# Kernel tuning notes

Measured on AMD Instinct MI355X. Metric: run time of the kernel, lower is better.

Reference implementation:

```python
import jax, jax.numpy as jnp
import numpy as np


def setup_inputs() -> dict:
    key = jax.random.key(0)
    k1, k2 = jax.random.split(key)
    B, L, D = 8, 2048, 128
    query = jax.random.normal(k1, (B, L, D), dtype=jnp.float32)
    value = jax.random.normal(k2, (B, L, D), dtype=jnp.float32)
    return {"query": query, "value": value}


def reference(query, value):
    # scores: [B, Lq, Lk] = query @ value^T (note: NO 1/sqrt(d) scaling, key == value)
    scores = jnp.einsum("bqd,bkd->bqk", query, value)
    weights = jax.nn.softmax(scores, axis=-1)
    # context: [B, Lq, D]
    context = jnp.einsum("bqk,bkd->bqd", weights, value)
    return context
```

## Files before the change

### kernel.cpp

```cpp
#include <hip/hip_runtime.h>
#include <hip/hip_fp16.h>

typedef _Float16 f16;
typedef __attribute__((ext_vector_type(8))) _Float16 f16x8;
typedef __attribute__((ext_vector_type(4))) _Float16 f16x4;
typedef __attribute__((ext_vector_type(4))) short s16x4;
typedef __attribute__((ext_vector_type(4))) float f32x4;
typedef __attribute__((ext_vector_type(2))) float f32x2;

#define MFMA16(a,b,c) __builtin_amdgcn_mfma_f32_16x16x32_f16(a,b,c,0,0,0)

#define B_DIM 8
#define L_DIM 2048
#define D_DIM 128
#define NGRP 4
#define KVB 64
#define NTILES 8
#define TILE_B 16384
#define P_ST 72
#define SLAB_ST 132
#define SMEM_B 137216

__device__ __forceinline__ unsigned ldsa(const void* p) {
    return (unsigned)(unsigned long long)(const __attribute__((address_space(3))) char*)p;
}

#define TRRD(d, a, O) asm volatile("ds_read_b64_tr_b16 %0, %1 offset:" O : "=v"(d) : "v"(a))
#define LGKM0() do { asm volatile("s_waitcnt lgkmcnt(0)" ::: "memory"); __builtin_amdgcn_sched_barrier(0); } while (0)

#define PVND(TL, TH, PA0, PA1, ND) { \
    union { s16x4 s2[2]; f16x8 v; } uu; uu.s2[0] = TL; uu.s2[1] = TH; \
    acc[0][ND] = MFMA16(PA0, uu.v, acc[0][ND]); \
    acc[1][ND] = MFMA16(PA1, uu.v, acc[1][ND]); }

#define PV_HALF(AREG, PA0, PA1, S0,S0b,S1,S1b,S2,S2b,S3,S3b, NDB) { \
    s16x4 t0l,t0h,t1l,t1h,t2l,t2h,t3l,t3h; \
    TRRD(t0l, AREG, S0);  TRRD(t0h, AREG, S0b); \
    TRRD(t1l, AREG, S1);  TRRD(t1h, AREG, S1b); \
    TRRD(t2l, AREG, S2);  TRRD(t2h, AREG, S2b); \
    TRRD(t3l, AREG, S3);  TRRD(t3h, AREG, S3b); \
    LGKM0(); \
    PVND(t0l, t0h, PA0, PA1, NDB+0); PVND(t1l, t1h, PA0, PA1, NDB+1); \
    PVND(t2l, t2h, PA0, PA1, NDB+2); PVND(t3l, t3h, PA0, PA1, NDB+3); }

__global__ __launch_bounds__(512, 2) void attn_fwd(
    const float* __restrict__ Q, const float* __restrict__ V, float* __restrict__ Out)
{
    __shared__ __align__(16) char smem[SMEM_B];

    const int tid  = threadIdx.x;
    const int wv   = tid >> 6;
    const int grp  = wv >> 1;
    const int qw   = wv & 1;
    const int lane = tid & 63;
    const int lrow = lane & 15;
    const int g    = lane >> 4;

    const int blk = blockIdx.x;
    const int b   = blk & 7;
    const int q0  = (blk >> 3) * 64;

    char* grpbase = smem + grp * (2 * TILE_B);

    f16x8 qhi[2][4], qlo[2][4];
    {
        const float* qb = Q + ((size_t)b * L_DIM + q0 + qw * 32) * D_DIM;
        #pragma unroll
        for (int q2 = 0; q2 < 2; ++q2) {
            const float* qp = qb + (size_t)(q2 * 16 + lrow) * D_DIM + g * 8;
            #pragma unroll
            for (int dt = 0; dt < 4; ++dt) {
                f32x4 f0 = *(const f32x4*)(qp + dt * 32);
                f32x4 f1 = *(const f32x4*)(qp + dt * 32 + 4);
                #pragma unroll
                for (int i = 0; i < 4; ++i) {
                    f16 h0 = (f16)f0[i];
                    qhi[q2][dt][i] = h0;
                    qlo[q2][dt][i] = (f16)(f0[i] - (float)h0);
                    f16 h1 = (f16)f1[i];
                    qhi[q2][dt][i + 4] = h1;
                    qlo[q2][dt][i + 4] = (f16)(f1[i] - (float)h1);
                }
            }
        }
    }

    f32x4 acc[2][8];
    #pragma unroll
    for (int q2 = 0; q2 < 2; ++q2)
        #pragma unroll
        for (int i = 0; i < 8; ++i) acc[q2][i] = (f32x4)0.0f;
    float m_run[2] = { -3.0e38f, -3.0e38f }, l_run[2] = { 0.0f, 0.0f };

    const int kvl = qw * 32 + (lane >> 3);
    const int d4l = lane & 7;
    const int gl_off = kvl * D_DIM + d4l * 4;
    const int wbase = ((kvl >> 2) * 1024) + ((d4l >> 2) * 128) + (kvl & 3) * 32 + (d4l & 3) * 8;
    const int qkoff = (lrow >> 2) * 1024 + (g >> 1) * 128 + (lrow & 3) * 32 + (g & 1) * 16;

    const float* vb = V + ((size_t)b * L_DIM + grp * (L_DIM / NGRP)) * D_DIM;

    {
        const float* vsrc = vb + gl_off;
        f32x4 ld0[16];
        #pragma unroll
        for (int ith = 0; ith < 4; ++ith)
            #pragma unroll
            for (int itd = 0; itd < 4; ++itd)
                ld0[ith * 4 + itd] = *(const f32x4*)(vsrc + ith * 1024 + itd * 32);
        #pragma unroll
        for (int ith = 0; ith < 4; ++ith)
            #pragma unroll
            for (int itd = 0; itd < 4; ++itd) {
                f32x4 f = ld0[ith * 4 + itd];
                f16x4 hv = { (f16)f[0], (f16)f[1], (f16)f[2], (f16)f[3] };
                *(f16x4*)(grpbase + wbase + ith * 2048 + itd * 256) = hv;
            }
    }
    __syncthreads();

    for (int t = 0; t < NTILES; ++t) {
        const int c = t & 1;
        char* cur = grpbase + c * TILE_B;
        char* alt = grpbase + (c ^ 1) * TILE_B;
        const bool hn = (t + 1 < NTILES);
        const float* vnext = vb + (size_t)(t + 1) * KVB * D_DIM + gl_off;

        f32x4 ldA[8], ldB[8];
        if (hn) {
            #pragma unroll
            for (int ith = 0; ith < 2; ++ith)
                #pragma unroll
                for (int itd = 0; itd < 4; ++itd)
                    ldA[ith * 4 + itd] = *(const f32x4*)(vnext + ith * 1024 + itd * 32);
        }

        f32x4 s[2][4];
        #pragma unroll
        for (int q2 = 0; q2 < 2; ++q2)
            #pragma unroll
            for (int nt = 0; nt < 4; ++nt) s[q2][nt] = (f32x4)0.0f;
        #pragma unroll
        for (int nt = 0; nt < 4; ++nt) {
            #pragma unroll
            for (int dt = 0; dt < 4; ++dt) {
                f16x8 a = *(const f16x8*)(cur + qkoff + nt * 4096 + dt * 256);
                s[0][nt] = MFMA16(a, qhi[0][dt], s[0][nt]);
                s[0][nt] = MFMA16(a, qlo[0][dt], s[0][nt]);
                s[1][nt] = MFMA16(a, qhi[1][dt], s[1][nt]);
                s[1][nt] = MFMA16(a, qlo[1][dt], s[1][nt]);
            }
        }

        if (hn) {
            #pragma unroll
            for (int ith = 0; ith < 2; ++ith)
                #pragma unroll
                for (int itd = 0; itd < 4; ++itd)
                    ldB[ith * 4 + itd] = *(const f32x4*)(vnext + (ith + 2) * 1024 + itd * 32);
        }

        float pm[2];
        #pragma unroll
        for (int q2 = 0; q2 < 2; ++q2) {
            float tm = s[q2][0][0];
            #pragma unroll
            for (int nt = 0; nt < 4; ++nt)
                #pragma unroll
                for (int r = 0; r < 4; ++r) tm = fmaxf(tm, s[q2][nt][r]);
            tm = fmaxf(tm, __shfl_xor(tm, 16));
            tm = fmaxf(tm, __shfl_xor(tm, 32));
            pm[q2] = tm;
        }
        bool need = (pm[0] > m_run[0] + 8.0f) || (pm[1] > m_run[1] + 8.0f);
        if (__any(need)) {
            float mnew[2], scl[2];
            #pragma unroll
            for (int q2 = 0; q2 < 2; ++q2) {
                mnew[q2] = fmaxf(m_run[q2], pm[q2]);
                scl[q2]  = __expf(m_run[q2] - mnew[q2]);
                m_run[q2] = mnew[q2];
                l_run[q2] *= scl[q2];
            }
            float sr[2][4];
            #pragma unroll
            for (int r = 0; r < 4; ++r) {
                sr[0][r] = __shfl(scl[0], g * 4 + r);
                sr[1][r] = __shfl(scl[1], g * 4 + r);
            }
            #pragma unroll
            for (int q2 = 0; q2 < 2; ++q2)
                #pragma unroll
                for (int nd = 0; nd < 8; ++nd)
                    #pragma unroll
                    for (int r = 0; r < 4; ++r) acc[q2][nd][r] *= sr[q2][r];
        }
        #pragma unroll
        for (int q2 = 0; q2 < 2; ++q2) {
            float ps = 0.0f;
            #pragma unroll
            for (int nt = 0; nt < 4; ++nt)
                #pragma unroll
                for (int r = 0; r < 4; ++r) {
                    float p = __expf(s[q2][nt][r] - m_run[q2]);
                    s[q2][nt][r] = p;
                    ps += p;
                }
            ps += __shfl_xor(ps, 16);
            ps += __shfl_xor(ps, 32);
            l_run[q2] += ps;
        }

        f16* pls = (f16*)(alt + qw * 8192);
        #pragma unroll
        for (int q2 = 0; q2 < 2; ++q2) {
            #pragma unroll
            for (int nt = 0; nt < 4; ++nt) {
                f16x4 w = { (f16)s[q2][nt][0], (f16)s[q2][nt][1],
                            (f16)s[q2][nt][2], (f16)s[q2][nt][3] };
                *(f16x4*)(pls + (size_t)(q2 * 16 + lrow) * P_ST + nt * 16 + g * 4) = w;
            }
        }
        f16x8 pa00, pa01, pa10, pa11;
        pa00 = *(const f16x8*)(pls + (size_t)(lrow) * P_ST + g * 8);
        pa01 = *(const f16x8*)(pls + (size_t)(lrow) * P_ST + 32 + g * 8);
        pa10 = *(const f16x8*)(pls + (size_t)(16 + lrow) * P_ST + g * 8);
        pa11 = *(const f16x8*)(pls + (size_t)(16 + lrow) * P_ST + 32 + g * 8);

        if (hn) {
            #pragma unroll
            for (int ith = 0; ith < 2; ++ith)
                #pragma unroll
                for (int itd = 0; itd < 4; ++itd) {
                    f32x4 f = ldA[ith * 4 + itd];
                    f16x4 hv = { (f16)f[0], (f16)f[1], (f16)f[2], (f16)f[3] };
                    *(f16x4*)(alt + wbase + ith * 2048 + itd * 256) = hv;
                }
        }

        unsigned atr0 = ldsa(cur) + (unsigned)(g * 2048 + lrow * 8);
        unsigned atr1 = atr0 + 8192u;
        PV_HALF(atr0, pa00, pa10, "0","1024","128","1152","256","1280","384","1408", 0);
        PV_HALF(atr0, pa00, pa10, "512","1536","640","1664","768","1792","896","1920", 4);
        PV_HALF(atr1, pa01, pa11, "0","1024","128","1152","256","1280","384","1408", 0);
        PV_HALF(atr1, pa01, pa11, "512","1536","640","1664","768","1792","896","1920", 4);

        if (hn) {
            #pragma unroll
            for (int ith = 0; ith < 2; ++ith)
                #pragma unroll
                for (int itd = 0; itd < 4; ++itd) {
                    f32x4 f = ldB[ith * 4 + itd];
                    f16x4 hv = { (f16)f[0], (f16)f[1], (f16)f[2], (f16)f[3] };
                    *(f16x4*)(alt + wbase + (ith + 2) * 2048 + itd * 256) = hv;
                }
        }
        __syncthreads();
    }

    float* slab = (float*)smem;
    float* mlp  = (float*)(smem + 8 * 32 * SLAB_ST * 4);
    #pragma unroll
    for (int q2 = 0; q2 < 2; ++q2)
        #pragma unroll
        for (int nd = 0; nd < 8; ++nd)
            #pragma unroll
            for (int r = 0; r < 4; ++r)
                slab[(size_t)(wv * 32 + q2 * 16 + g * 4 + r) * SLAB_ST + nd * 16 + lrow] = acc[q2][nd][r];
    if (g == 0) {
        #pragma unroll
        for (int q2 = 0; q2 < 2; ++q2) {
            mlp[wv * 64 + q2 * 16 + lrow]      = m_run[q2];
            mlp[wv * 64 + 32 + q2 * 16 + lrow] = l_run[q2];
        }
    }
    __syncthreads();

    #pragma unroll
    for (int rr = 0; rr < 8; ++rr) {
        int row = wv * 8 + rr;
        int qws = row >> 5, ql = row & 31;
        float mg[4], M = -3.0e38f;
        #pragma unroll
        for (int gg = 0; gg < 4; ++gg) {
            mg[gg] = mlp[(gg * 2 + qws) * 64 + ql];
            M = fmaxf(M, mg[gg]);
        }
        float L = 0.0f, f[4];
        #pragma unroll
        for (int gg = 0; gg < 4; ++gg) {
            f[gg] = __expf(mg[gg] - M);
            L += f[gg] * mlp[(gg * 2 + qws) * 64 + 32 + ql];
        }
        float inv = 1.0f / L;
        f32x2 o = { 0.0f, 0.0f };
        #pragma unroll
        for (int gg = 0; gg < 4; ++gg) {
            f32x2 v = *(const f32x2*)&slab[(size_t)((gg * 2 + qws) * 32 + ql) * SLAB_ST + lane * 2];
            o[0] += f[gg] * v[0];
            o[1] += f[gg] * v[1];
        }
        o[0] *= inv; o[1] *= inv;
        *(f32x2*)&Out[((size_t)b * L_DIM + q0 + row) * D_DIM + lane * 2] = o;
    }
}

extern "C" void kernel_launch(void* const* d_in, const int* in_sizes, int n_in,
                              void* d_out, int out_size, void* d_ws, size_t ws_size,
                              hipStream_t stream) {
    const float* Q = (const float*)d_in[0];
    const float* V = (const float*)d_in[1];
    float* Out     = (float*)d_out;
    attn_fwd<<<dim3(B_DIM * (L_DIM / 64)), dim3(512), 0, stream>>>(Q, V, Out);
}
```

Before: 45.59 us.

## Pad LDS tile blocks, fold log2e into Q, raise MFMA priority

```diff
diff --git a/kernel.cpp b/kernel.cpp
--- a/kernel.cpp
+++ b/kernel.cpp
@@ -9,6 +9,8 @@
 typedef __attribute__((ext_vector_type(2))) float f32x2;
 
 #define MFMA16(a,b,c) __builtin_amdgcn_mfma_f32_16x16x32_f16(a,b,c,0,0,0)
+#define EXP2(x) __builtin_amdgcn_exp2f(x)
+#define LOG2E 1.4426950408889634f
 
 #define B_DIM 8
 #define L_DIM 2048
@@ -16,7 +18,8 @@
 #define NGRP 4
 #define KVB 64
 #define NTILES 8
-#define TILE_B 16384
+#define BLKB 1040
+#define TILE_B (16 * BLKB)
 #define P_ST 72
 #define SLAB_ST 132
 #define SMEM_B 137216
@@ -40,8 +43,10 @@
     TRRD(t2l, AREG, S2);  TRRD(t2h, AREG, S2b); \
     TRRD(t3l, AREG, S3);  TRRD(t3h, AREG, S3b); \
     LGKM0(); \
+    __builtin_amdgcn_s_setprio(1); \
     PVND(t0l, t0h, PA0, PA1, NDB+0); PVND(t1l, t1h, PA0, PA1, NDB+1); \
-    PVND(t2l, t2h, PA0, PA1, NDB+2); PVND(t3l, t3h, PA0, PA1, NDB+3); }
+    PVND(t2l, t2h, PA0, PA1, NDB+2); PVND(t3l, t3h, PA0, PA1, NDB+3); \
+    __builtin_amdgcn_s_setprio(0); }
 
 __global__ __launch_bounds__(512, 2) void attn_fwd(
     const float* __restrict__ Q, const float* __restrict__ V, float* __restrict__ Out)
@@ -74,12 +79,14 @@
                 f32x4 f1 = *(const f32x4*)(qp + dt * 32 + 4);
                 #pragma unroll
                 for (int i = 0; i < 4; ++i) {
-                    f16 h0 = (f16)f0[i];
+                    float s0 = f0[i] * LOG2E;
+                    f16 h0 = (f16)s0;
                     qhi[q2][dt][i] = h0;
-                    qlo[q2][dt][i] = (f16)(f0[i] - (float)h0);
-                    f16 h1 = (f16)f1[i];
+                    qlo[q2][dt][i] = (f16)(s0 - (float)h0);
+                    float s1 = f1[i] * LOG2E;
+                    f16 h1 = (f16)s1;
                     qhi[q2][dt][i + 4] = h1;
-                    qlo[q2][dt][i + 4] = (f16)(f1[i] - (float)h1);
+                    qlo[q2][dt][i + 4] = (f16)(s1 - (float)h1);
                 }
             }
         }
@@ -95,8 +102,8 @@
     const int kvl = qw * 32 + (lane >> 3);
     const int d4l = lane & 7;
     const int gl_off = kvl * D_DIM + d4l * 4;
-    const int wbase = ((kvl >> 2) * 1024) + ((d4l >> 2) * 128) + (kvl & 3) * 32 + (d4l & 3) * 8;
-    const int qkoff = (lrow >> 2) * 1024 + (g >> 1) * 128 + (lrow & 3) * 32 + (g & 1) * 16;
+    const int wbase = ((kvl >> 2) * BLKB) + ((d4l >> 2) * 128) + (kvl & 3) * 32 + (d4l & 3) * 8;
+    const int qkoff = (lrow >> 2) * BLKB + (g >> 1) * 128 + (lrow & 3) * 32 + (g & 1) * 16;
 
     const float* vb = V + ((size_t)b * L_DIM + grp * (L_DIM / NGRP)) * D_DIM;
 
@@ -114,7 +121,7 @@
             for (int itd = 0; itd < 4; ++itd) {
                 f32x4 f = ld0[ith * 4 + itd];
                 f16x4 hv = { (f16)f[0], (f16)f[1], (f16)f[2], (f16)f[3] };
-                *(f16x4*)(grpbase + wbase + ith * 2048 + itd * 256) = hv;
+                *(f16x4*)(grpbase + wbase + ith * (2 * BLKB) + itd * 256) = hv;
             }
     }
     __syncthreads();
@@ -140,17 +147,19 @@
         for (int q2 = 0; q2 < 2; ++q2)
             #pragma unroll
             for (int nt = 0; nt < 4; ++nt) s[q2][nt] = (f32x4)0.0f;
+        __builtin_amdgcn_s_setprio(1);
         #pragma unroll
         for (int nt = 0; nt < 4; ++nt) {
             #pragma unroll
             for (int dt = 0; dt < 4; ++dt) {
-                f16x8 a = *(const f16x8*)(cur + qkoff + nt * 4096 + dt * 256);
+                f16x8 a = *(const f16x8*)(cur + qkoff + nt * (4 * BLKB) + dt * 256);
                 s[0][nt] = MFMA16(a, qhi[0][dt], s[0][nt]);
                 s[0][nt] = MFMA16(a, qlo[0][dt], s[0][nt]);
                 s[1][nt] = MFMA16(a, qhi[1][dt], s[1][nt]);
                 s[1][nt] = MFMA16(a, qlo[1][dt], s[1][nt]);
             }
         }
+        __builtin_amdgcn_s_setprio(0);
 
         if (hn) {
             #pragma unroll
@@ -172,14 +181,14 @@
             tm = fmaxf(tm, __shfl_xor(tm, 32));
             pm[q2] = tm;
         }
-        bool need = (pm[0] > m_run[0] + 8.0f) || (pm[1] > m_run[1] + 8.0f);
+        bool need = (pm[0] > m_run[0] + 11.5f) || (pm[1] > m_run[1] + 11.5f);
         if (__any(need)) {
-            float mnew[2], scl[2];
+            float scl[2];
             #pragma unroll
             for (int q2 = 0; q2 < 2; ++q2) {
-                mnew[q2] = fmaxf(m_run[q2], pm[q2]);
-                scl[q2]  = __expf(m_run[q2] - mnew[q2]);
-                m_run[q2] = mnew[q2];
+                float mnew = fmaxf(m_run[q2], pm[q2]);
+                scl[q2]  = EXP2(m_run[q2] - mnew);
+                m_run[q2] = mnew;
                 l_run[q2] *= scl[q2];
             }
             float sr[2][4];
@@ -202,7 +211,7 @@
             for (int nt = 0; nt < 4; ++nt)
                 #pragma unroll
                 for (int r = 0; r < 4; ++r) {
-                    float p = __expf(s[q2][nt][r] - m_run[q2]);
+                    float p = EXP2(s[q2][nt][r] - m_run[q2]);
                     s[q2][nt][r] = p;
                     ps += p;
                 }
@@ -211,7 +220,7 @@
             l_run[q2] += ps;
         }
 
-        f16* pls = (f16*)(alt + qw * 8192);
+        f16* pls = (f16*)(alt + qw * (8 * BLKB));
         #pragma unroll
         for (int q2 = 0; q2 < 2; ++q2) {
             #pragma unroll
@@ -234,16 +243,16 @@
                 for (int itd = 0; itd < 4; ++itd) {
                     f32x4 f = ldA[ith * 4 + itd];
                     f16x4 hv = { (f16)f[0], (f16)f[1], (f16)f[2], (f16)f[3] };
-                    *(f16x4*)(alt + wbase + ith * 2048 + itd * 256) = hv;
+                    *(f16x4*)(alt + wbase + ith * (2 * BLKB) + itd * 256) = hv;
                 }
         }
 
-        unsigned atr0 = ldsa(cur) + (unsigned)(g * 2048 + lrow * 8);
-        unsigned atr1 = atr0 + 8192u;
-        PV_HALF(atr0, pa00, pa10, "0","1024","128","1152","256","1280","384","1408", 0);
-        PV_HALF(atr0, pa00, pa10, "512","1536","640","1664","768","1792","896","1920", 4);
-        PV_HALF(atr1, pa01, pa11, "0","1024","128","1152","256","1280","384","1408", 0);
-        PV_HALF(atr1, pa01, pa11, "512","1536","640","1664","768","1792","896","1920", 4);
+        unsigned atr0 = ldsa(cur) + (unsigned)(g * (2 * BLKB) + lrow * 8);
+        unsigned atr1 = atr0 + (unsigned)(8 * BLKB);
+        PV_HALF(atr0, pa00, pa10, "0","1040","128","1168","256","1296","384","1424", 0);
+        PV_HALF(atr0, pa00, pa10, "512","1552","640","1680","768","1808","896","1936", 4);
+        PV_HALF(atr1, pa01, pa11, "0","1040","128","1168","256","1296","384","1424", 0);
+        PV_HALF(atr1, pa01, pa11, "512","1552","640","1680","768","1808","896","1936", 4);
 
         if (hn) {
             #pragma unroll
@@ -252,7 +261,7 @@
                 for (int itd = 0; itd < 4; ++itd) {
                     f32x4 f = ldB[ith * 4 + itd];
                     f16x4 hv = { (f16)f[0], (f16)f[1], (f16)f[2], (f16)f[3] };
-                    *(f16x4*)(alt + wbase + (ith + 2) * 2048 + itd * 256) = hv;
+                    *(f16x4*)(alt + wbase + (ith + 2) * (2 * BLKB) + itd * 256) = hv;
                 }
         }
         __syncthreads();
@@ -289,7 +298,7 @@
         float L = 0.0f, f[4];
         #pragma unroll
         for (int gg = 0; gg < 4; ++gg) {
-            f[gg] = __expf(mg[gg] - M);
+            f[gg] = EXP2(mg[gg] - M);
             L += f[gg] * mlp[(gg * 2 + qws) * 64 + 32 + ql];
         }
         float inv = 1.0f / L;
```

New measurement: 45.08 us. Within noise of the previous version (-1.1%).
